# Kernel optimization log

Measured on AMD Instinct MI355X. Metric: run time of the kernel, lower is better.

Reference implementation:

```python
import jax, jax.numpy as jnp
import numpy as np


def setup_inputs() -> dict:
    key = jax.random.key(0)
    k1, k2, k3, k4 = jax.random.split(key, 4)
    B, S, D = 4, 2048, 1024
    return {
        "x": jax.random.normal(k1, (B, S, D), dtype=jnp.float32),
        "wq": jax.random.normal(k2, (D, D), dtype=jnp.float32),
        "wk": jax.random.normal(k3, (D, D), dtype=jnp.float32),
        "wv": jax.random.normal(k4, (D, D), dtype=jnp.float32),
    }


def reference(x, wq, wk, wv):
    # q,k,v: [B,S,D]
    q = x @ wq
    k = x @ wk
    v = x @ wv
    # NOTE: source applies NO 1/sqrt(d) scaling; we match it faithfully.
    scores = jnp.einsum("bsd,btd->bst", q, k)  # [B,S,S]
    weights = jax.nn.softmax(scores, axis=-1)
    return jnp.einsum("bst,btd->bsd", weights, v)  # [B,S,D]
```

## Files before the change

### kernel.cpp

```cpp
#include <hip/hip_runtime.h>


typedef _Float16 half4_t __attribute__((ext_vector_type(4)));
typedef _Float16 half8_t __attribute__((ext_vector_type(8)));
typedef float f32x4 __attribute__((ext_vector_type(4)));

#define BM 128
#define BN 128
#define BK 32

__device__ __forceinline__ void gl_lds16(const _Float16* g, _Float16* l) {
    __builtin_amdgcn_global_load_lds(
        (const __attribute__((address_space(1))) unsigned int*)g,
        (__attribute__((address_space(3))) unsigned int*)l, 16, 0, 0);
}

__global__ __launch_bounds__(256) void conv_all_kernel(
    const float* __restrict__ x, const float* __restrict__ wq,
    const float* __restrict__ wk, const float* __restrict__ wv,
    _Float16* __restrict__ xh, _Float16* __restrict__ xl,
    _Float16* __restrict__ qh, _Float16* __restrict__ ql,
    _Float16* __restrict__ kh, _Float16* __restrict__ kl,
    _Float16* __restrict__ vTh)
{
    __shared__ float tle[64][65];
    const int bid = blockIdx.x;
    if (bid < 10240) {
        const float* in;
        _Float16 *hi, *lo;
        int i0;
        if (bid < 8192)      { in = x;  hi = xh; lo = xl; i0 = bid; }
        else if (bid < 9216) { in = wq; hi = qh; lo = ql; i0 = bid - 8192; }
        else                 { in = wk; hi = kh; lo = kl; i0 = bid - 9216; }
        int i = i0 * 256 + threadIdx.x;
        float4 v = ((const float4*)in)[i];
        float xs[4] = {v.x, v.y, v.z, v.w};
        half4_t h, l;
#pragma unroll
        for (int j = 0; j < 4; ++j) {
            _Float16 hh = (_Float16)xs[j];
            h[j] = hh;
            l[j] = (_Float16)(xs[j] - (float)hh);
        }
        ((half4_t*)hi)[i] = h;
        ((half4_t*)lo)[i] = l;
    } else {
        const int t = bid - 10240;
        const int tr = (t >> 4) * 64, tc = (t & 15) * 64;
        const int t16 = threadIdx.x & 15, tq = threadIdx.x >> 4;
#pragma unroll
        for (int j = 0; j < 4; ++j) {
            int lr = tq + j * 16;
            float4 v = *(const float4*)(wv + (size_t)(tr + lr) * 1024 + tc + t16 * 4);
            tle[lr][t16 * 4 + 0] = v.x;
            tle[lr][t16 * 4 + 1] = v.y;
            tle[lr][t16 * 4 + 2] = v.z;
            tle[lr][t16 * 4 + 3] = v.w;
        }
        __syncthreads();
#pragma unroll
        for (int j = 0; j < 4; ++j) {
            int orow = tq + j * 16;
            int oc = t16 * 4;
            half4_t h;
#pragma unroll
            for (int i = 0; i < 4; ++i) h[i] = (_Float16)tle[oc + i][orow];
            *(half4_t*)(vTh + (size_t)(tc + orow) * 1024 + tr + oc) = h;
        }
    }
}

template <bool OUTF32>
__global__ __launch_bounds__(256) void gemm_split(
    const _Float16* __restrict__ Ah, const _Float16* __restrict__ Al, size_t az,
    const _Float16* __restrict__ Bh, const _Float16* __restrict__ Bl, size_t bz,
    float* __restrict__ Cf, size_t cz, int ldc,
    _Float16* __restrict__ Oh, _Float16* __restrict__ Ol, size_t oz, int ldo,
    int lda, int ldb, int K)
{
    __shared__ __align__(16) _Float16 sAh[BM][BK], sAl[BM][BK];
    __shared__ __align__(16) _Float16 sBh[BN][BK], sBl[BN][BK];

    const int tid = threadIdx.x;
    const int wave = tid >> 6, lane = tid & 63;
    const int wm = (wave >> 1) * 64, wn = (wave & 1) * 64;
    const int lrow = lane & 15, quad = lane >> 4;
    const int bm = blockIdx.y * BM, bn = blockIdx.x * BN;
    const int z = blockIdx.z;

    const _Float16* pAh = Ah + (size_t)z * az;
    const _Float16* pAl = Al + (size_t)z * az;
    const _Float16* pBh = Bh + (size_t)z * bz;
    const _Float16* pBl = Bl + (size_t)z * bz;

    const int r0 = wave * 32 + (lane >> 2);
    const int kofs = (lane & 3) * 8;
    const size_t a0o = (size_t)(bm + r0) * lda + kofs;
    const size_t a1o = a0o + (size_t)16 * lda;
    const size_t b0o = (size_t)(bn + r0) * ldb + kofs;
    const size_t b1o = b0o + (size_t)16 * ldb;
    _Float16* lA0 = &sAh[r0][kofs];
    _Float16* lA1 = &sAh[r0 + 16][kofs];
    _Float16* lAl0 = &sAl[r0][kofs];
    _Float16* lAl1 = &sAl[r0 + 16][kofs];
    _Float16* lB0 = &sBh[r0][kofs];
    _Float16* lB1 = &sBh[r0 + 16][kofs];
    _Float16* lBl0 = &sBl[r0][kofs];
    _Float16* lBl1 = &sBl[r0 + 16][kofs];

    f32x4 acc[4][4];
#pragma unroll
    for (int i = 0; i < 4; ++i)
#pragma unroll
        for (int j = 0; j < 4; ++j) acc[i][j] = 0.0f;

    for (int k0 = 0; k0 < K; k0 += BK) {
        gl_lds16(pAh + a0o + k0, lA0);
        gl_lds16(pAh + a1o + k0, lA1);
        gl_lds16(pAl + a0o + k0, lAl0);
        gl_lds16(pAl + a1o + k0, lAl1);
        gl_lds16(pBh + b0o + k0, lB0);
        gl_lds16(pBh + b1o + k0, lB1);
        gl_lds16(pBl + b0o + k0, lBl0);
        gl_lds16(pBl + b1o + k0, lBl1);
        __syncthreads();

        half8_t a0[4], a1[4], b0[4], b1[4];
#pragma unroll
        for (int mt = 0; mt < 4; ++mt) {
            a0[mt] = *(const half8_t*)&sAh[wm + mt * 16 + lrow][quad * 8];
            a1[mt] = *(const half8_t*)&sAl[wm + mt * 16 + lrow][quad * 8];
        }
#pragma unroll
        for (int nt = 0; nt < 4; ++nt) {
            b0[nt] = *(const half8_t*)&sBh[wn + nt * 16 + lrow][quad * 8];
            b1[nt] = *(const half8_t*)&sBl[wn + nt * 16 + lrow][quad * 8];
        }
#pragma unroll
        for (int mt = 0; mt < 4; ++mt)
#pragma unroll
            for (int nt = 0; nt < 4; ++nt) {
                acc[mt][nt] = __builtin_amdgcn_mfma_f32_16x16x32_f16(a0[mt], b0[nt], acc[mt][nt], 0, 0, 0);
                acc[mt][nt] = __builtin_amdgcn_mfma_f32_16x16x32_f16(a0[mt], b1[nt], acc[mt][nt], 0, 0, 0);
                acc[mt][nt] = __builtin_amdgcn_mfma_f32_16x16x32_f16(a1[mt], b0[nt], acc[mt][nt], 0, 0, 0);
            }
        __syncthreads();
    }

#pragma unroll
    for (int mt = 0; mt < 4; ++mt)
#pragma unroll
        for (int nt = 0; nt < 4; ++nt)
#pragma unroll
            for (int r = 0; r < 4; ++r) {
                int gm = bm + wm + mt * 16 + quad * 4 + r;
                int gn = bn + wn + nt * 16 + lrow;
                float v = acc[mt][nt][r];
                if (OUTF32) {
                    Cf[(size_t)z * cz + (size_t)gm * ldc + gn] = v;
                } else {
                    _Float16 h = (_Float16)v;
                    Oh[(size_t)z * oz + (size_t)gm * ldo + gn] = h;
                    Ol[(size_t)z * oz + (size_t)gm * ldo + gn] = (_Float16)(v - (float)h);
                }
            }
}

#define NTILES 48

__global__ __launch_bounds__(512, 2) void scores_8ph(
    const _Float16* __restrict__ yh, const _Float16* __restrict__ yl,
    const _Float16* __restrict__ xh, const _Float16* __restrict__ xl,
    float* __restrict__ Cf)
{
    __shared__ __align__(16) _Float16 sA[4][8192];
    __shared__ __align__(16) _Float16 sB[4][8192];

    const int tid = threadIdx.x;
    const int wave = tid >> 6, lane = tid & 63;
    const int wm = (wave >> 2) * 128;
    const int wn = (wave & 3) * 64;
    const int l15 = lane & 15, jq = lane >> 4;

    const int flat = blockIdx.x + (blockIdx.y << 3) + (blockIdx.z << 6);
    const int work = ((flat & 7) << 5) + (flat >> 3);
    const int z = work >> 6;
    const int bm = ((work >> 3) & 7) * 256;
    const int bn = (work & 7) * 256;

    const _Float16* Ah = yh + ((size_t)z * 2048 + bm) * 1024;
    const _Float16* Al = yl + ((size_t)z * 2048 + bm) * 1024;
    const _Float16* Bh = xh + ((size_t)z * 2048 + bn) * 1024;
    const _Float16* Bl = xl + ((size_t)z * 2048 + bn) * 1024;

    int a_off[8], b_off[4];
#pragma unroll
    for (int h = 0; h < 2; ++h)
#pragma unroll
        for (int m = 0; m < 4; ++m) {
            int row = wm + h * 64 + m * 16 + l15;
            int F = row * 4 + (jq ^ ((row >> 1) & 3));
            a_off[h * 4 + m] = F * 16;
            asm volatile("" : "+v"(a_off[h * 4 + m]));
        }
#pragma unroll
    for (int n = 0; n < 4; ++n) {
        int row = wn + n * 16 + l15;
        int F = row * 4 + (jq ^ ((row >> 1) & 3));
        b_off[n] = F * 16;
        asm volatile("" : "+v"(b_off[n]));
    }
    int row0 = tid >> 2;
    int j0 = (tid & 3) ^ ((row0 >> 1) & 3);
    int g0 = row0 * 2048 + j0 * 16;
    int g1 = g0 + 262144;
    asm volatile("" : "+v"(g0), "+v"(g1));

    _Float16* SA0 = sA[0]; _Float16* SA1 = sA[1];
    _Float16* SA2 = sA[2]; _Float16* SA3 = sA[3];
    _Float16* SB0 = sB[0]; _Float16* SB1 = sB[1];
    _Float16* SB2 = sB[2]; _Float16* SB3 = sB[3];

    auto STG = [&](const _Float16* p, _Float16* slot) {
        gl_lds16((const _Float16*)((const char*)p + g0), slot + tid * 8);
        gl_lds16((const _Float16*)((const char*)p + g1), slot + 4096 + tid * 8);
    };
    auto APAN = [&](int tt, int kh) {
        return (tt < 32 ? Ah : Al) + (tt & 15) * 64 + kh * 32;
    };
    auto BPAN = [&](int tt, int kh) {
        return ((tt >> 4) == 1 ? Bl : Bh) + (tt & 15) * 64 + kh * 32;
    };
    auto RDA = [&](const _Float16* slot, int half, half8_t* dst) {
#pragma unroll
        for (int m = 0; m < 4; ++m)
            dst[m] = *(const half8_t*)((const char*)slot + a_off[half * 4 + m]);
    };
    auto RDB = [&](const _Float16* slot, half8_t* dst) {
#pragma unroll
        for (int n = 0; n < 4; ++n)
            dst[n] = *(const half8_t*)((const char*)slot + b_off[n]);
    };

    f32x4 acc[8][4];
#pragma unroll
    for (int i = 0; i < 8; ++i)
#pragma unroll
        for (int j = 0; j < 4; ++j) acc[i][j] = 0.0f;

    auto MM = [&](half8_t* aa, half8_t* bb, int ah) {
#pragma unroll
        for (int m = 0; m < 4; ++m)
#pragma unroll
            for (int n = 0; n < 4; ++n)
                acc[ah * 4 + m][n] = __builtin_amdgcn_mfma_f32_16x16x32_f16(
                    aa[m], bb[n], acc[ah * 4 + m][n], 0, 0, 0);
    };

#define BARRIER __builtin_amdgcn_s_barrier()
#define LGKM0   asm volatile("s_waitcnt lgkmcnt(0)")
#define VM4     asm volatile("s_waitcnt vmcnt(4)")
#define P1      __builtin_amdgcn_s_setprio(1)
#define P0      __builtin_amdgcn_s_setprio(0)

    STG(APAN(0, 0), SA0); STG(BPAN(0, 0), SB0);
    STG(APAN(0, 1), SA1); STG(BPAN(0, 1), SB1);
    STG(APAN(1, 0), SA2); STG(BPAN(1, 0), SB2);
    VM4;
    BARRIER;

    for (int t = 0; t < NTILES; t += 2) {
        const int u1 = t + 1;
        const int u2 = (t + 2 < NTILES) ? t + 2 : NTILES - 1;
        const int u3 = (t + 3 < NTILES) ? t + 3 : NTILES - 1;
        half8_t aa[4], bb[4];

        RDB(SB0, bb); RDA(SA0, 0, aa); STG(APAN(u1, 1), SA3);
        BARRIER; LGKM0; P1; MM(aa, bb, 0); P0; BARRIER;

        RDA(SA0, 1, aa); STG(BPAN(u1, 1), SB3);
        BARRIER; LGKM0; P1; MM(aa, bb, 1); P0; BARRIER;

        RDB(SB1, bb); RDA(SA1, 0, aa); STG(APAN(u2, 0), SA0);
        BARRIER; LGKM0; P1; MM(aa, bb, 0); P0; BARRIER;

        RDA(SA1, 1, aa); STG(BPAN(u2, 0), SB0);
        BARRIER; LGKM0; P1; MM(aa, bb, 1); P0; VM4; BARRIER;

        RDB(SB2, bb); RDA(SA2, 0, aa); STG(APAN(u2, 1), SA1);
        BARRIER; LGKM0; P1; MM(aa, bb, 0); P0; BARRIER;

        RDA(SA2, 1, aa); STG(BPAN(u2, 1), SB1);
        BARRIER; LGKM0; P1; MM(aa, bb, 1); P0; BARRIER;

        RDB(SB3, bb); RDA(SA3, 0, aa); STG(APAN(u3, 0), SA2);
        BARRIER; LGKM0; P1; MM(aa, bb, 0); P0; BARRIER;

        RDA(SA3, 1, aa); STG(BPAN(u3, 0), SB2);
        BARRIER; LGKM0; P1; MM(aa, bb, 1); P0; VM4; BARRIER;
    }
    asm volatile("s_waitcnt vmcnt(0)");

#undef BARRIER
#undef LGKM0
#undef VM4
#undef P1
#undef P0

    float* C = Cf + (size_t)z * 2048 * 2048;
#pragma unroll
    for (int mi = 0; mi < 8; ++mi)
#pragma unroll
        for (int ni = 0; ni < 4; ++ni) {
            int gm0 = bm + wm + mi * 16 + jq * 4;
            int gn = bn + wn + ni * 16 + l15;
#pragma unroll
            for (int r = 0; r < 4; ++r)
                C[(size_t)(gm0 + r) * 2048 + gn] = acc[mi][ni][r];
        }
}

__global__ __launch_bounds__(256) void yv_kernel(
    const _Float16* __restrict__ xh, const _Float16* __restrict__ xl,
    const _Float16* __restrict__ Mh, const _Float16* __restrict__ Ml,
    const _Float16* __restrict__ wvTh,
    _Float16* __restrict__ yh, _Float16* __restrict__ yl,
    _Float16* __restrict__ vT)
{
    __shared__ __align__(16) char buf[128 * 132 * 2];

    const int tid = threadIdx.x;
    const int wave = tid >> 6, lane = tid & 63;
    const int wm = (wave >> 1) * 64, wn = (wave & 1) * 64;
    const int lrow = lane & 15, quad = lane >> 4;
    const int bm = blockIdx.y * BM, bn = blockIdx.x * BN;
    const bool vrole = (blockIdx.z != 0);

    const int r0 = wave * 32 + (lane >> 2);
    const int kofs = (lane & 3) * 8;
    const size_t a0o = (size_t)(bm + r0) * 1024 + kofs;
    const size_t a1o = a0o + (size_t)16 * 1024;
    const size_t b0o = (size_t)(bn + r0) * 1024 + kofs;
    const size_t b1o = b0o + (size_t)16 * 1024;

    f32x4 acc[4][4];
#pragma unroll
    for (int i = 0; i < 4; ++i)
#pragma unroll
        for (int j = 0; j < 4; ++j) acc[i][j] = 0.0f;

    _Float16* tle = (_Float16*)buf;

    if (!vrole) {
        _Float16* sAh = (_Float16*)buf;
        _Float16* sAl = (_Float16*)(buf + 8192);
        _Float16* sBh = (_Float16*)(buf + 16384);
        _Float16* sBl = (_Float16*)(buf + 24576);
        _Float16* lA0 = sAh + r0 * BK + kofs;
        _Float16* lA1 = sAh + (r0 + 16) * BK + kofs;
        _Float16* lAl0 = sAl + r0 * BK + kofs;
        _Float16* lAl1 = sAl + (r0 + 16) * BK + kofs;
        _Float16* lB0 = sBh + r0 * BK + kofs;
        _Float16* lB1 = sBh + (r0 + 16) * BK + kofs;
        _Float16* lBl0 = sBl + r0 * BK + kofs;
        _Float16* lBl1 = sBl + (r0 + 16) * BK + kofs;

        for (int k0 = 0; k0 < 1024; k0 += BK) {
            gl_lds16(xh + a0o + k0, lA0);
            gl_lds16(xh + a1o + k0, lA1);
            gl_lds16(xl + a0o + k0, lAl0);
            gl_lds16(xl + a1o + k0, lAl1);
            gl_lds16(Mh + b0o + k0, lB0);
            gl_lds16(Mh + b1o + k0, lB1);
            gl_lds16(Ml + b0o + k0, lBl0);
            gl_lds16(Ml + b1o + k0, lBl1);
            __syncthreads();

            half8_t a0[4], a1[4], b0[4], b1[4];
#pragma unroll
            for (int mt = 0; mt < 4; ++mt) {
                a0[mt] = *(const half8_t*)(sAh + (wm + mt * 16 + lrow) * BK + quad * 8);
                a1[mt] = *(const half8_t*)(sAl + (wm + mt * 16 + lrow) * BK + quad * 8);
            }
#pragma unroll
            for (int nt = 0; nt < 4; ++nt) {
                b0[nt] = *(const half8_t*)(sBh + (wn + nt * 16 + lrow) * BK + quad * 8);
                b1[nt] = *(const half8_t*)(sBl + (wn + nt * 16 + lrow) * BK + quad * 8);
            }
#pragma unroll
            for (int mt = 0; mt < 4; ++mt)
#pragma unroll
                for (int nt = 0; nt < 4; ++nt) {
                    acc[mt][nt] = __builtin_amdgcn_mfma_f32_16x16x32_f16(a0[mt], b0[nt], acc[mt][nt], 0, 0, 0);
                    acc[mt][nt] = __builtin_amdgcn_mfma_f32_16x16x32_f16(a0[mt], b1[nt], acc[mt][nt], 0, 0, 0);
                    acc[mt][nt] = __builtin_amdgcn_mfma_f32_16x16x32_f16(a1[mt], b0[nt], acc[mt][nt], 0, 0, 0);
                }
            __syncthreads();
        }

#pragma unroll
        for (int pass = 0; pass < 2; ++pass) {
            if (pass) __syncthreads();
#pragma unroll
            for (int mt = 0; mt < 4; ++mt)
#pragma unroll
                for (int nt = 0; nt < 4; ++nt) {
                    int rloc = wm + mt * 16 + quad * 4;
                    int cloc = wn + nt * 16 + lrow;
#pragma unroll
                    for (int r = 0; r < 4; ++r) {
                        float v = acc[mt][nt][r];
                        _Float16 h = (_Float16)v;
                        tle[(rloc + r) * 132 + cloc] =
                            pass == 0 ? h : (_Float16)(v - (float)h);
                    }
                }
            __syncthreads();
            _Float16* dst = pass == 0 ? yh : yl;
#pragma unroll
            for (int i = 0; i < 8; ++i) {
                int flat = i * 256 + tid;
                int rloc = flat >> 4, c = (flat & 15) * 8;
                half8_t o8;
#pragma unroll
                for (int j = 0; j < 8; ++j) o8[j] = tle[rloc * 132 + c + j];
                *(half8_t*)(dst + (size_t)(bm + rloc) * 1024 + bn + c) = o8;
            }
        }
    } else {
        _Float16* sA = (_Float16*)buf;
        _Float16* sB = (_Float16*)(buf + 8192);
        _Float16* lA0 = sA + r0 * BK + kofs;
        _Float16* lA1 = sA + (r0 + 16) * BK + kofs;
        _Float16* lB0 = sB + r0 * BK + kofs;
        _Float16* lB1 = sB + (r0 + 16) * BK + kofs;

        for (int k0 = 0; k0 < 1024; k0 += BK) {
            gl_lds16(xh + a0o + k0, lA0);
            gl_lds16(xh + a1o + k0, lA1);
            gl_lds16(wvTh + b0o + k0, lB0);
            gl_lds16(wvTh + b1o + k0, lB1);
            __syncthreads();

            half8_t a0[4], b0[4];
#pragma unroll
            for (int mt = 0; mt < 4; ++mt)
                a0[mt] = *(const half8_t*)(sA + (wm + mt * 16 + lrow) * BK + quad * 8);
#pragma unroll
            for (int nt = 0; nt < 4; ++nt)
                b0[nt] = *(const half8_t*)(sB + (wn + nt * 16 + lrow) * BK + quad * 8);
#pragma unroll
            for (int mt = 0; mt < 4; ++mt)
#pragma unroll
                for (int nt = 0; nt < 4; ++nt)
                    acc[mt][nt] = __builtin_amdgcn_mfma_f32_16x16x32_f16(a0[mt], b0[nt], acc[mt][nt], 0, 0, 0);
            __syncthreads();
        }

#pragma unroll
        for (int mt = 0; mt < 4; ++mt)
#pragma unroll
            for (int nt = 0; nt < 4; ++nt) {
                int t0 = wm + mt * 16 + quad * 4;
                int e_l = wn + nt * 16 + lrow;
                half4_t o;
#pragma unroll
                for (int r = 0; r < 4; ++r) o[r] = (_Float16)acc[mt][nt][r];
                *(half4_t*)(tle + e_l * 132 + t0) = o;
            }
        __syncthreads();
        const int b = bm >> 11, tb = bm & 2047;
#pragma unroll
        for (int i = 0; i < 8; ++i) {
            int flat = i * 256 + tid;
            int e_l = flat >> 4, c = (flat & 15) * 8;
            half8_t o8;
#pragma unroll
            for (int j = 0; j < 8; ++j) o8[j] = tle[e_l * 132 + c + j];
            *(half8_t*)(vT + ((size_t)b << 21) + (size_t)(bn + e_l) * 2048 + tb + c) = o8;
        }
    }
}

__global__ __launch_bounds__(256) void gemm_plain(
    const _Float16* __restrict__ Ag, size_t az,
    const _Float16* __restrict__ Bg, size_t bz,
    float* __restrict__ Cf, size_t cz, int ldc,
    int lda, int ldb, int K)
{
    __shared__ __align__(16) _Float16 sA[BM][BK], sB[BN][BK];

    const int tid = threadIdx.x;
    const int wave = tid >> 6, lane = tid & 63;
    const int wm = (wave >> 1) * 64, wn = (wave & 1) * 64;
    const int lrow = lane & 15, quad = lane >> 4;
    const int bm = blockIdx.y * BM, bn = blockIdx.x * BN;
    const int z = blockIdx.z;

    const _Float16* pA = Ag + (size_t)z * az;
    const _Float16* pB = Bg + (size_t)z * bz;

    const int r0 = wave * 32 + (lane >> 2);
    const int kofs = (lane & 3) * 8;
    const size_t a0o = (size_t)(bm + r0) * lda + kofs;
    const size_t a1o = a0o + (size_t)16 * lda;
    const size_t b0o = (size_t)(bn + r0) * ldb + kofs;
    const size_t b1o = b0o + (size_t)16 * ldb;
    _Float16* lA0 = &sA[r0][kofs];
    _Float16* lA1 = &sA[r0 + 16][kofs];
    _Float16* lB0 = &sB[r0][kofs];
    _Float16* lB1 = &sB[r0 + 16][kofs];

    f32x4 acc[4][4];
#pragma unroll
    for (int i = 0; i < 4; ++i)
#pragma unroll
        for (int j = 0; j < 4; ++j) acc[i][j] = 0.0f;

    for (int k0 = 0; k0 < K; k0 += BK) {
        gl_lds16(pA + a0o + k0, lA0);
        gl_lds16(pA + a1o + k0, lA1);
        gl_lds16(pB + b0o + k0, lB0);
        gl_lds16(pB + b1o + k0, lB1);
        __syncthreads();

        half8_t a0[4], b0[4];
#pragma unroll
        for (int mt = 0; mt < 4; ++mt)
            a0[mt] = *(const half8_t*)&sA[wm + mt * 16 + lrow][quad * 8];
#pragma unroll
        for (int nt = 0; nt < 4; ++nt)
            b0[nt] = *(const half8_t*)&sB[wn + nt * 16 + lrow][quad * 8];
#pragma unroll
        for (int mt = 0; mt < 4; ++mt)
#pragma unroll
            for (int nt = 0; nt < 4; ++nt)
                acc[mt][nt] = __builtin_amdgcn_mfma_f32_16x16x32_f16(a0[mt], b0[nt], acc[mt][nt], 0, 0, 0);
        __syncthreads();
    }

#pragma unroll
    for (int mt = 0; mt < 4; ++mt)
#pragma unroll
        for (int nt = 0; nt < 4; ++nt) {
            int gm0 = bm + wm + mt * 16 + quad * 4;
            int gn = bn + wn + nt * 16 + lrow;
#pragma unroll
            for (int r = 0; r < 4; ++r)
                Cf[(size_t)z * cz + (size_t)(gm0 + r) * ldc + gn] = acc[mt][nt][r];
        }
}

__global__ __launch_bounds__(256) void softmax_kernel(float* __restrict__ S)
{
    float* row = S + (size_t)blockIdx.x * 2048;
    float4* r4 = (float4*)row;
    const int tid = threadIdx.x;
    const int wave = tid >> 6, lane = tid & 63;

    float4 a = r4[tid], b = r4[tid + 256];
    float m = fmaxf(fmaxf(fmaxf(a.x, a.y), fmaxf(a.z, a.w)),
                    fmaxf(fmaxf(b.x, b.y), fmaxf(b.z, b.w)));
#pragma unroll
    for (int o = 32; o; o >>= 1) m = fmaxf(m, __shfl_xor(m, o));
    __shared__ float redm[4];
    __shared__ float reds[4];
    if (lane == 0) redm[wave] = m;
    __syncthreads();
    m = fmaxf(fmaxf(redm[0], redm[1]), fmaxf(redm[2], redm[3]));

    a.x = __expf(a.x - m); a.y = __expf(a.y - m);
    a.z = __expf(a.z - m); a.w = __expf(a.w - m);
    b.x = __expf(b.x - m); b.y = __expf(b.y - m);
    b.z = __expf(b.z - m); b.w = __expf(b.w - m);

    float s = a.x + a.y + a.z + a.w + b.x + b.y + b.z + b.w;
#pragma unroll
    for (int o = 32; o; o >>= 1) s += __shfl_xor(s, o);
    if (lane == 0) reds[wave] = s;
    __syncthreads();
    s = reds[0] + reds[1] + reds[2] + reds[3];

    float inv = 1.0f / s;
    _Float16* o16 = (_Float16*)row;
    half4_t ha, hb;
    ha[0] = (_Float16)(a.x * inv); ha[1] = (_Float16)(a.y * inv);
    ha[2] = (_Float16)(a.z * inv); ha[3] = (_Float16)(a.w * inv);
    hb[0] = (_Float16)(b.x * inv); hb[1] = (_Float16)(b.y * inv);
    hb[2] = (_Float16)(b.z * inv); hb[3] = (_Float16)(b.w * inv);
    ((half4_t*)o16)[tid] = ha;
    ((half4_t*)o16)[tid + 256] = hb;
}

extern "C" void kernel_launch(void* const* d_in, const int* in_sizes, int n_in,
                              void* d_out, int out_size, void* d_ws, size_t ws_size,
                              hipStream_t stream)
{
    const float* x  = (const float*)d_in[0];
    const float* wq = (const float*)d_in[1];
    const float* wk = (const float*)d_in[2];
    const float* wv = (const float*)d_in[3];
    float* out = (float*)d_out;

    const int S = 2048, D = 1024;
    char* ws = (char*)d_ws;

    _Float16* xh   = (_Float16*)(ws);
    _Float16* xl   = (_Float16*)(ws + (16ull << 20));
    _Float16* yh   = (_Float16*)(ws + (32ull << 20));
    _Float16* yl   = (_Float16*)(ws + (48ull << 20));
    _Float16* vT   = (_Float16*)(ws + (64ull << 20));
    _Float16* wqh  = (_Float16*)(ws + (80ull << 20));
    _Float16* wql  = (_Float16*)(ws + (82ull << 20));
    _Float16* wkh  = (_Float16*)(ws + (84ull << 20));
    _Float16* wkl  = (_Float16*)(ws + (86ull << 20));
    _Float16* wvTh = (_Float16*)(ws + (88ull << 20));
    _Float16* Mh   = (_Float16*)(ws + (90ull << 20));
    _Float16* Ml   = (_Float16*)(ws + (92ull << 20));
    float*    sc   = (float*)(ws + (94ull << 20));

    conv_all_kernel<<<dim3(10496), dim3(256), 0, stream>>>(
        x, wq, wk, wv, xh, xl, wqh, wql, wkh, wkl, wvTh);

    gemm_split<false><<<dim3(D / BN, D / BM, 1), dim3(256), 0, stream>>>(
        wkh, wkl, 0, wqh, wql, 0, nullptr, 0, 0, Mh, Ml, 0, D, D, D, D);

    yv_kernel<<<dim3(D / BN, 8192 / BM, 2), dim3(256), 0, stream>>>(
        xh, xl, Mh, Ml, wvTh, yh, yl, vT);

    scores_8ph<<<dim3(S / 256, S / 256, 4), dim3(512), 0, stream>>>(
        yh, yl, xh, xl, sc);

    softmax_kernel<<<dim3(4 * S), dim3(256), 0, stream>>>(sc);

    gemm_plain<<<dim3(D / BN, S / BM, 4), dim3(256), 0, stream>>>(
        (const _Float16*)sc, (size_t)S * 4096, vT, (size_t)D * S,
        out, (size_t)S * D, D, 4096, S, S);
}
```

Before: 402.0 us.

## Stage GEMM tiles through registers instead of direct global-to-LDS loads

```diff
diff --git a/kernel.cpp b/kernel.cpp
--- a/kernel.cpp
+++ b/kernel.cpp
@@ -214,16 +214,24 @@
     int j0 = (tid & 3) ^ ((row0 >> 1) & 3);
     int g0 = row0 * 2048 + j0 * 16;
     int g1 = g0 + 262144;
-    asm volatile("" : "+v"(g0), "+v"(g1));
+    int wb0 = tid * 16;
+    int wb1 = 8192 + tid * 16;
+    asm volatile("" : "+v"(g0), "+v"(g1), "+v"(wb0), "+v"(wb1));
 
     _Float16* SA0 = sA[0]; _Float16* SA1 = sA[1];
     _Float16* SA2 = sA[2]; _Float16* SA3 = sA[3];
     _Float16* SB0 = sB[0]; _Float16* SB1 = sB[1];
     _Float16* SB2 = sB[2]; _Float16* SB3 = sB[3];
 
-    auto STG = [&](const _Float16* p, _Float16* slot) {
-        gl_lds16((const _Float16*)((const char*)p + g0), slot + tid * 8);
-        gl_lds16((const _Float16*)((const char*)p + g1), slot + 4096 + tid * 8);
+    f32x4 rAk0[2], rBk0[2], rAk1[2], rBk1[2];
+
+    auto ISSUE = [&](const _Float16* p, f32x4* r) {
+        r[0] = *(const f32x4*)((const char*)p + g0);
+        r[1] = *(const f32x4*)((const char*)p + g1);
+    };
+    auto WRITE = [&](const f32x4* r, _Float16* slot) {
+        *(f32x4*)((char*)slot + wb0) = r[0];
+        *(f32x4*)((char*)slot + wb1) = r[1];
     };
     auto APAN = [&](int tt, int kh) {
         return (tt < 32 ? Ah : Al) + (tt & 15) * 64 + kh * 32;
@@ -259,51 +267,59 @@
 
 #define BARRIER __builtin_amdgcn_s_barrier()
 #define LGKM0   asm volatile("s_waitcnt lgkmcnt(0)")
-#define VM4     asm volatile("s_waitcnt vmcnt(4)")
 #define P1      __builtin_amdgcn_s_setprio(1)
 #define P0      __builtin_amdgcn_s_setprio(0)
 
-    STG(APAN(0, 0), SA0); STG(BPAN(0, 0), SB0);
-    STG(APAN(0, 1), SA1); STG(BPAN(0, 1), SB1);
-    STG(APAN(1, 0), SA2); STG(BPAN(1, 0), SB2);
-    VM4;
+    ISSUE(APAN(0, 0), rAk0); ISSUE(BPAN(0, 0), rBk0);
+    ISSUE(APAN(0, 1), rAk1); ISSUE(BPAN(0, 1), rBk1);
+    WRITE(rAk0, SA0); WRITE(rBk0, SB0);
+    WRITE(rAk1, SA1); WRITE(rBk1, SB1);
+    ISSUE(APAN(1, 0), rAk0); ISSUE(BPAN(1, 0), rBk0);
+    WRITE(rAk0, SA2); WRITE(rBk0, SB2);
+    ISSUE(APAN(1, 1), rAk1); ISSUE(BPAN(1, 1), rBk1);
+    LGKM0;
     BARRIER;
 
     for (int t = 0; t < NTILES; t += 2) {
-        const int u1 = t + 1;
         const int u2 = (t + 2 < NTILES) ? t + 2 : NTILES - 1;
         const int u3 = (t + 3 < NTILES) ? t + 3 : NTILES - 1;
         half8_t aa[4], bb[4];
 
-        RDB(SB0, bb); RDA(SA0, 0, aa); STG(APAN(u1, 1), SA3);
+        RDB(SB0, bb); RDA(SA0, 0, aa);
+        WRITE(rAk1, SA3); ISSUE(APAN(u2, 0), rAk0);
         BARRIER; LGKM0; P1; MM(aa, bb, 0); P0; BARRIER;
 
-        RDA(SA0, 1, aa); STG(BPAN(u1, 1), SB3);
+        RDA(SA0, 1, aa);
+        WRITE(rBk1, SB3); ISSUE(BPAN(u2, 0), rBk0);
         BARRIER; LGKM0; P1; MM(aa, bb, 1); P0; BARRIER;
 
-        RDB(SB1, bb); RDA(SA1, 0, aa); STG(APAN(u2, 0), SA0);
+        RDB(SB1, bb); RDA(SA1, 0, aa);
+        WRITE(rAk0, SA0); ISSUE(APAN(u2, 1), rAk1);
         BARRIER; LGKM0; P1; MM(aa, bb, 0); P0; BARRIER;
 
-        RDA(SA1, 1, aa); STG(BPAN(u2, 0), SB0);
-        BARRIER; LGKM0; P1; MM(aa, bb, 1); P0; VM4; BARRIER;
-
-        RDB(SB2, bb); RDA(SA2, 0, aa); STG(APAN(u2, 1), SA1);
+        RDA(SA1, 1, aa);
+        WRITE(rBk0, SB0); ISSUE(BPAN(u2, 1), rBk1);
+        BARRIER; LGKM0; P1; MM(aa, bb, 1); P0; BARRIER;
+
+        RDB(SB2, bb); RDA(SA2, 0, aa);
+        WRITE(rAk1, SA1); ISSUE(APAN(u3, 0), rAk0);
         BARRIER; LGKM0; P1; MM(aa, bb, 0); P0; BARRIER;
 
-        RDA(SA2, 1, aa); STG(BPAN(u2, 1), SB1);
+        RDA(SA2, 1, aa);
+        WRITE(rBk1, SB1); ISSUE(BPAN(u3, 0), rBk0);
         BARRIER; LGKM0; P1; MM(aa, bb, 1); P0; BARRIER;
 
-        RDB(SB3, bb); RDA(SA3, 0, aa); STG(APAN(u3, 0), SA2);
+        RDB(SB3, bb); RDA(SA3, 0, aa);
+        WRITE(rAk0, SA2); ISSUE(APAN(u3, 1), rAk1);
         BARRIER; LGKM0; P1; MM(aa, bb, 0); P0; BARRIER;
 
-        RDA(SA3, 1, aa); STG(BPAN(u3, 0), SB2);
-        BARRIER; LGKM0; P1; MM(aa, bb, 1); P0; VM4; BARRIER;
+        RDA(SA3, 1, aa);
+        WRITE(rBk0, SB2); ISSUE(BPAN(u3, 1), rBk1);
+        BARRIER; LGKM0; P1; MM(aa, bb, 1); P0; BARRIER;
     }
-    asm volatile("s_waitcnt vmcnt(0)");
 
 #undef BARRIER
 #undef LGKM0
-#undef VM4
 #undef P1
 #undef P0
 
```

Measured after the change: 393.8 us. 1.02x faster.

## Stage GEMM tiles through registers with double-buffered fragment prefetch

Applied to the files above, without the earlier changes.

```diff
diff --git a/kernel.cpp b/kernel.cpp
--- a/kernel.cpp
+++ b/kernel.cpp
@@ -193,37 +193,45 @@
     const _Float16* Bh = xh + ((size_t)z * 2048 + bn) * 1024;
     const _Float16* Bl = xl + ((size_t)z * 2048 + bn) * 1024;
 
-    int a_off[8], b_off[4];
-#pragma unroll
-    for (int h = 0; h < 2; ++h)
-#pragma unroll
-        for (int m = 0; m < 4; ++m) {
-            int row = wm + h * 64 + m * 16 + l15;
-            int F = row * 4 + (jq ^ ((row >> 1) & 3));
-            a_off[h * 4 + m] = F * 16;
-            asm volatile("" : "+v"(a_off[h * 4 + m]));
-        }
-#pragma unroll
-    for (int n = 0; n < 4; ++n) {
-        int row = wn + n * 16 + l15;
+    int a_off0, b_off0;
+    {
+        int row = wm + l15;
         int F = row * 4 + (jq ^ ((row >> 1) & 3));
-        b_off[n] = F * 16;
-        asm volatile("" : "+v"(b_off[n]));
+        a_off0 = F * 16;
+        row = wn + l15;
+        F = row * 4 + (jq ^ ((row >> 1) & 3));
+        b_off0 = F * 16;
     }
+    asm volatile("" : "+v"(a_off0), "+v"(b_off0));
     int row0 = tid >> 2;
     int j0 = (tid & 3) ^ ((row0 >> 1) & 3);
     int g0 = row0 * 2048 + j0 * 16;
     int g1 = g0 + 262144;
-    asm volatile("" : "+v"(g0), "+v"(g1));
+    int wb0 = tid * 16;
+    asm volatile("" : "+v"(g0), "+v"(g1), "+v"(wb0));
 
     _Float16* SA0 = sA[0]; _Float16* SA1 = sA[1];
     _Float16* SA2 = sA[2]; _Float16* SA3 = sA[3];
     _Float16* SB0 = sB[0]; _Float16* SB1 = sB[1];
     _Float16* SB2 = sB[2]; _Float16* SB3 = sB[3];
 
-    auto STG = [&](const _Float16* p, _Float16* slot) {
-        gl_lds16((const _Float16*)((const char*)p + g0), slot + tid * 8);
-        gl_lds16((const _Float16*)((const char*)p + g1), slot + 4096 + tid * 8);
+    f32x4 rA[2], rB[2];
+
+    auto ISSUEA = [&](const _Float16* p) {
+        rA[0] = *(const f32x4*)((const char*)p + g0);
+        rA[1] = *(const f32x4*)((const char*)p + g1);
+    };
+    auto ISSUEB = [&](const _Float16* p) {
+        rB[0] = *(const f32x4*)((const char*)p + g0);
+        rB[1] = *(const f32x4*)((const char*)p + g1);
+    };
+    auto WRA = [&](_Float16* slot) {
+        *(f32x4*)((char*)slot + wb0) = rA[0];
+        *(f32x4*)((char*)slot + wb0 + 8192) = rA[1];
+    };
+    auto WRB = [&](_Float16* slot) {
+        *(f32x4*)((char*)slot + wb0) = rB[0];
+        *(f32x4*)((char*)slot + wb0 + 8192) = rB[1];
     };
     auto APAN = [&](int tt, int kh) {
         return (tt < 32 ? Ah : Al) + (tt & 15) * 64 + kh * 32;
@@ -234,12 +242,13 @@
     auto RDA = [&](const _Float16* slot, int half, half8_t* dst) {
 #pragma unroll
         for (int m = 0; m < 4; ++m)
-            dst[m] = *(const half8_t*)((const char*)slot + a_off[half * 4 + m]);
+            dst[m] = *(const half8_t*)((const char*)slot + a_off0 +
+                                       half * 4096 + m * 1024);
     };
     auto RDB = [&](const _Float16* slot, half8_t* dst) {
 #pragma unroll
         for (int n = 0; n < 4; ++n)
-            dst[n] = *(const half8_t*)((const char*)slot + b_off[n]);
+            dst[n] = *(const half8_t*)((const char*)slot + b_off0 + n * 1024);
     };
 
     f32x4 acc[8][4];
@@ -258,52 +267,49 @@
     };
 
 #define BARRIER __builtin_amdgcn_s_barrier()
-#define LGKM0   asm volatile("s_waitcnt lgkmcnt(0)")
-#define VM4     asm volatile("s_waitcnt vmcnt(4)")
 #define P1      __builtin_amdgcn_s_setprio(1)
 #define P0      __builtin_amdgcn_s_setprio(0)
 
-    STG(APAN(0, 0), SA0); STG(BPAN(0, 0), SB0);
-    STG(APAN(0, 1), SA1); STG(BPAN(0, 1), SB1);
-    STG(APAN(1, 0), SA2); STG(BPAN(1, 0), SB2);
-    VM4;
-    BARRIER;
+    half8_t aa0[4], aa1[4], bb0v[4], bb1v[4];
+
+    ISSUEA(APAN(0, 0)); ISSUEB(BPAN(0, 0)); WRA(SA0); WRB(SB0);
+    ISSUEA(APAN(0, 1)); ISSUEB(BPAN(0, 1)); WRA(SA1); WRB(SB1);
+    ISSUEA(APAN(1, 0)); ISSUEB(BPAN(1, 0)); WRA(SA2); WRB(SB2);
+    ISSUEA(APAN(1, 1));
+    __syncthreads();
+    RDB(SB0, bb0v); RDA(SA0, 0, aa0);
 
     for (int t = 0; t < NTILES; t += 2) {
         const int u1 = t + 1;
         const int u2 = (t + 2 < NTILES) ? t + 2 : NTILES - 1;
         const int u3 = (t + 3 < NTILES) ? t + 3 : NTILES - 1;
-        half8_t aa[4], bb[4];
-
-        RDB(SB0, bb); RDA(SA0, 0, aa); STG(APAN(u1, 1), SA3);
-        BARRIER; LGKM0; P1; MM(aa, bb, 0); P0; BARRIER;
-
-        RDA(SA0, 1, aa); STG(BPAN(u1, 1), SB3);
-        BARRIER; LGKM0; P1; MM(aa, bb, 1); P0; BARRIER;
-
-        RDB(SB1, bb); RDA(SA1, 0, aa); STG(APAN(u2, 0), SA0);
-        BARRIER; LGKM0; P1; MM(aa, bb, 0); P0; BARRIER;
-
-        RDA(SA1, 1, aa); STG(BPAN(u2, 0), SB0);
-        BARRIER; LGKM0; P1; MM(aa, bb, 1); P0; VM4; BARRIER;
-
-        RDB(SB2, bb); RDA(SA2, 0, aa); STG(APAN(u2, 1), SA1);
-        BARRIER; LGKM0; P1; MM(aa, bb, 0); P0; BARRIER;
-
-        RDA(SA2, 1, aa); STG(BPAN(u2, 1), SB1);
-        BARRIER; LGKM0; P1; MM(aa, bb, 1); P0; BARRIER;
-
-        RDB(SB3, bb); RDA(SA3, 0, aa); STG(APAN(u3, 0), SA2);
-        BARRIER; LGKM0; P1; MM(aa, bb, 0); P0; BARRIER;
-
-        RDA(SA3, 1, aa); STG(BPAN(u3, 0), SB2);
-        BARRIER; LGKM0; P1; MM(aa, bb, 1); P0; VM4; BARRIER;
+
+        RDA(SA0, 1, aa1); WRA(SA3); ISSUEB(BPAN(u1, 1));
+        BARRIER; P1; MM(aa0, bb0v, 0); P0;
+
+        RDB(SB1, bb1v); RDA(SA1, 0, aa0); WRB(SB3); ISSUEA(APAN(u2, 0));
+        BARRIER; P1; MM(aa1, bb0v, 1); P0;
+
+        RDA(SA1, 1, aa1); WRA(SA0); ISSUEB(BPAN(u2, 0));
+        BARRIER; P1; MM(aa0, bb1v, 0); P0;
+
+        RDB(SB2, bb0v); RDA(SA2, 0, aa0); WRB(SB0); ISSUEA(APAN(u2, 1));
+        BARRIER; P1; MM(aa1, bb1v, 1); P0;
+
+        RDA(SA2, 1, aa1); WRA(SA1); ISSUEB(BPAN(u2, 1));
+        BARRIER; P1; MM(aa0, bb0v, 0); P0;
+
+        RDB(SB3, bb1v); RDA(SA3, 0, aa0); WRB(SB1); ISSUEA(APAN(u3, 0));
+        BARRIER; P1; MM(aa1, bb0v, 1); P0;
+
+        RDA(SA3, 1, aa1); WRA(SA2); ISSUEB(BPAN(u3, 0));
+        BARRIER; P1; MM(aa0, bb1v, 0); P0;
+
+        RDB(SB0, bb0v); RDA(SA0, 0, aa0); WRB(SB2); ISSUEA(APAN(u3, 1));
+        BARRIER; P1; MM(aa1, bb1v, 1); P0;
     }
-    asm volatile("s_waitcnt vmcnt(0)");
 
 #undef BARRIER
-#undef LGKM0
-#undef VM4
 #undef P1
 #undef P0
 
```

Result: no change. 396.0 us (-1.5%).
